# Performance work log

Measured on AMD Instinct MI355X. Metric: run time of the kernel, lower is better.

The kernel has to match this reference:

```python
import jax, jax.numpy as jnp
import numpy as np
import math

N, S, T, D = 4, 2048, 2048, 1024

def setup_inputs() -> dict:
    key = jax.random.key(0)
    ks = jax.random.split(key, 6)
    scale = 1.0 / math.sqrt(D)
    return {
        "query": jax.random.normal(ks[0], (N, S, D), dtype=jnp.float32),
        "key": jax.random.normal(ks[1], (N, T, D), dtype=jnp.float32),
        "value": jax.random.normal(ks[2], (N, T, D), dtype=jnp.float32),
        # causal mask: 1 = attend, 0 = masked out (masked_fill where mask == 0)
        "attn_mask": jnp.tril(jnp.ones((S, T), dtype=jnp.int32)),
        "Wq": jax.random.normal(ks[3], (D, D), dtype=jnp.float32) * scale,
        "Wk": jax.random.normal(ks[4], (D, D), dtype=jnp.float32) * scale,
        "Wv": jax.random.normal(ks[5], (D, D), dtype=jnp.float32) * scale,
    }

def reference(query, key, value, attn_mask, Wq, Wk, Wv):
    # nn.Linear(bias=False): y = x @ W.T
    q = jnp.einsum('nsd,ed->nse', query, Wq)
    k = jnp.einsum('ntd,ed->nte', key, Wk)
    v = jnp.einsum('ntd,ed->nte', value, Wv)
    # scaled dot-product scores [N, S, T]
    dot = jnp.einsum('nse,nte->nst', q, k) / jnp.sqrt(jnp.asarray(D, q.dtype))
    dot = jnp.where(attn_mask == 0, -jnp.inf, dot)
    scores = jax.nn.softmax(dot, axis=-1)
    # dropout is identity in eval mode
    y = jnp.einsum('nst,nte->nse', scores, v)
    return y
```

## Files before the change

kernel.cpp:

```cpp
#include <hip/hip_runtime.h>
#include <math.h>

using u16 = unsigned short;
typedef __attribute__((ext_vector_type(8))) __bf16 bf16x8;
typedef __attribute__((ext_vector_type(4))) float f32x4;
typedef __attribute__((ext_vector_type(4))) float f4v;
typedef __attribute__((ext_vector_type(8))) u16 u16x8;

__device__ __forceinline__ u16 f2bf(float f) {
  unsigned u = __float_as_uint(f);
  u += 0x7fffu + ((u >> 16) & 1u);
  return (u16)(u >> 16);
}

__device__ __forceinline__ void gload16(const void* g, void* l) {
  __builtin_amdgcn_global_load_lds(
      (const __attribute__((address_space(1))) unsigned int*)g,
      (__attribute__((address_space(3))) unsigned int*)l, 16, 0, 0);
}

__global__ __launch_bounds__(256) void cast3_f32_bf16(
    const float* __restrict__ p0, const float* __restrict__ p1,
    const float* __restrict__ p2, u16* __restrict__ out, size_t ostride) {
  int z = blockIdx.z;
  const float* in = (z == 0) ? p0 : (z == 1) ? p1 : p2;
  size_t i = ((size_t)blockIdx.x * 256 + threadIdx.x) * 8;
  f4v a = *reinterpret_cast<const f4v*>(in + i);
  f4v b = *reinterpret_cast<const f4v*>(in + i + 4);
  u16x8 r;
  r[0] = f2bf(a[0]); r[1] = f2bf(a[1]); r[2] = f2bf(a[2]); r[3] = f2bf(a[3]);
  r[4] = f2bf(b[0]); r[5] = f2bf(b[1]); r[6] = f2bf(b[2]); r[7] = f2bf(b[3]);
  *reinterpret_cast<u16x8*>(out + z * ostride + i) = r;
}

__global__ __launch_bounds__(256) void transpose_bf16k(const u16* __restrict__ in,
                                                       u16* __restrict__ out) {
  __shared__ u16 t[64][65];
  int c0 = blockIdx.x * 64, r0 = blockIdx.y * 64;
  size_t zb = (size_t)blockIdx.z * 2048 * 1024;
  const u16* I = in + zb;
  u16* O = out + zb;
  int tx = threadIdx.x & 63, ty = threadIdx.x >> 6;
  #pragma unroll
  for (int i = 0; i < 64; i += 4)
    t[ty + i][tx] = I[(size_t)(r0 + ty + i) * 1024 + c0 + tx];
  __syncthreads();
  #pragma unroll
  for (int i = 0; i < 64; i += 4)
    O[(size_t)(c0 + ty + i) * 2048 + r0 + tx] = t[tx][ty + i];
}

#define BM 128
#define BN 128
#define BK 32

template<typename OutT, int MODE>
__global__ __launch_bounds__(256) void gemm_bt(
    const u16* __restrict__ A, const u16* __restrict__ B, OutT* __restrict__ C,
    int K, int lda, int ldb, int ldc,
    size_t sA, size_t sB, size_t sC, float alpha,
    OutT* __restrict__ C1, OutT* __restrict__ C2) {
  int bn, bm, bz = 0;
  int kEnd = K;
  const u16* Ag;
  const u16* Bg;
  OutT* Cg;

  if (MODE == 3) {
    int h = blockIdx.x;
    int l = (h & 7) * 192 + (h >> 3);
    bn = l & 7;
    int bm192 = l >> 3;
    int which = bm192 >> 6;
    bm = bm192 & 63;
    Ag = A + (size_t)which * sA + (size_t)bm * BM * lda;
    Bg = B + (size_t)which * sB + (size_t)bn * BN * ldb;
    Cg = (which == 0) ? C : (which == 1) ? C1 : C2;
  } else if (MODE == 1) {
    int h = blockIdx.x;
    int l = (h & 7) * 68 + (h >> 3);
    bz = l / 136;
    int t = l % 136;
    bm = (int)((sqrtf(8.f * (float)t + 1.f) - 1.f) * 0.5f);
    while ((bm + 1) * (bm + 2) / 2 <= t) ++bm;
    while (bm * (bm + 1) / 2 > t) --bm;
    bn = t - bm * (bm + 1) / 2;
    Ag = A + sA * bz + (size_t)bm * BM * lda;
    Bg = B + sB * bz + (size_t)bn * BN * ldb;
    Cg = C + sC * bz;
  } else {
    int l = blockIdx.x;
    bm = 15 - (l >> 5);
    int rest = l & 31;
    bz = rest >> 3;
    bn = rest & 7;
    kEnd = (K < (bm + 1) * BM) ? K : (bm + 1) * BM;
    Ag = A + sA * bz + (size_t)bm * BM * lda;
    Bg = B + sB * bz + (size_t)bn * BN * ldb;
    Cg = C + sC * bz;
  }

  __shared__ __align__(16) u16 As[2][BM * BK];
  __shared__ __align__(16) u16 Bs[2][BN * BK];

  const int tid = threadIdx.x;
  const int lane = tid & 63, wave = tid >> 6;
  const int wr = wave >> 1, wc = wave & 1;

  const int ch0 = wave, ch1 = wave + 4;
  const int e0 = ch0 * 512 + lane * 8, e1 = ch1 * 512 + lane * 8;
  const int r0 = e0 >> 5, c0 = e0 & 31, r1 = e1 >> 5, c1 = e1 & 31;
  const u16* a0 = Ag + (size_t)r0 * lda + c0;
  const u16* a1 = Ag + (size_t)r1 * lda + c1;
  const u16* b0 = Bg + (size_t)r0 * ldb + c0;
  const u16* b1 = Bg + (size_t)r1 * ldb + c1;

  f32x4 acc[4][4] = {};

  const int fr = lane & 15, kq = (lane >> 4) * 8;
  const int nt = kEnd / BK;

  gload16(a0, &As[0][ch0 * 512]);
  gload16(a1, &As[0][ch1 * 512]);
  gload16(b0, &Bs[0][ch0 * 512]);
  gload16(b1, &Bs[0][ch1 * 512]);
  __syncthreads();

  for (int t = 0; t < nt; ++t) {
    const int cur = t & 1;
    if (t + 1 < nt) {
      const int k0 = (t + 1) * BK;
      gload16(a0 + k0, &As[cur ^ 1][ch0 * 512]);
      gload16(a1 + k0, &As[cur ^ 1][ch1 * 512]);
      gload16(b0 + k0, &Bs[cur ^ 1][ch0 * 512]);
      gload16(b1 + k0, &Bs[cur ^ 1][ch1 * 512]);
    }
    bf16x8 af[4], bfv[4];
    #pragma unroll
    for (int m = 0; m < 4; ++m)
      af[m] = *reinterpret_cast<const bf16x8*>(&As[cur][(wr * 64 + m * 16 + fr) * BK + kq]);
    #pragma unroll
    for (int n = 0; n < 4; ++n)
      bfv[n] = *reinterpret_cast<const bf16x8*>(&Bs[cur][(wc * 64 + n * 16 + fr) * BK + kq]);
    #pragma unroll
    for (int m = 0; m < 4; ++m)
      #pragma unroll
      for (int n = 0; n < 4; ++n)
        acc[m][n] = __builtin_amdgcn_mfma_f32_16x16x32_bf16(af[m], bfv[n], acc[m][n], 0, 0, 0);
    __syncthreads();
  }

  const int row0 = bm * BM + wr * 64 + (lane >> 4) * 4;
  const int col0 = bn * BN + wc * 64 + fr;
  #pragma unroll
  for (int m = 0; m < 4; ++m)
    #pragma unroll
    for (int n = 0; n < 4; ++n) {
      #pragma unroll
      for (int j = 0; j < 4; ++j) {
        float val = acc[m][n][j] * alpha;
        size_t idx = (size_t)(row0 + m * 16 + j) * ldc + (col0 + n * 16);
        if constexpr (sizeof(OutT) == 2) Cg[idx] = f2bf(val);
        else Cg[idx] = val;
      }
    }
}

__global__ __launch_bounds__(256) void softmax_causal(float* __restrict__ sc) {
  int r = blockIdx.x;
  int s = r & 2047;
  float* row = sc + (size_t)r * 2048;
  int tid = threadIdx.x;
  int t0 = tid * 8;
  f4v x0 = {-1e30f, -1e30f, -1e30f, -1e30f};
  f4v x1 = {-1e30f, -1e30f, -1e30f, -1e30f};
  if (t0 <= s)     x0 = reinterpret_cast<const f4v*>(row)[tid * 2];
  if (t0 + 4 <= s) x1 = reinterpret_cast<const f4v*>(row)[tid * 2 + 1];
  float v[8] = {x0[0], x0[1], x0[2], x0[3], x1[0], x1[1], x1[2], x1[3]};
  float mx = -1e30f;
  #pragma unroll
  for (int j = 0; j < 8; ++j) {
    v[j] = ((t0 + j) <= s) ? v[j] : -1e30f;
    mx = fmaxf(mx, v[j]);
  }
  #pragma unroll
  for (int o = 32; o; o >>= 1) mx = fmaxf(mx, __shfl_xor(mx, o, 64));
  __shared__ float red[8];
  if ((tid & 63) == 0) red[tid >> 6] = mx;
  __syncthreads();
  mx = fmaxf(fmaxf(red[0], red[1]), fmaxf(red[2], red[3]));
  float p[8];
  float sum = 0.f;
  #pragma unroll
  for (int j = 0; j < 8; ++j) {
    p[j] = ((t0 + j) <= s) ? __expf(v[j] - mx) : 0.f;
    sum += p[j];
  }
  #pragma unroll
  for (int o = 32; o; o >>= 1) sum += __shfl_xor(sum, o, 64);
  if ((tid & 63) == 0) red[4 + (tid >> 6)] = sum;
  __syncthreads();
  sum = red[4] + red[5] + red[6] + red[7];
  float inv = 1.0f / sum;
  u16x8 o8;
  #pragma unroll
  for (int j = 0; j < 8; ++j) o8[j] = f2bf(p[j] * inv);
  if (t0 <= (s | 127))
    reinterpret_cast<u16x8*>(row)[tid] = o8;
}

extern "C" void kernel_launch(void* const* d_in, const int* in_sizes, int n_in,
                              void* d_out, int out_size, void* d_ws, size_t ws_size,
                              hipStream_t stream) {
  const float* q  = (const float*)d_in[0];
  const float* k  = (const float*)d_in[1];
  const float* v  = (const float*)d_in[2];
  const float* Wq = (const float*)d_in[4];
  const float* Wk = (const float*)d_in[5];
  const float* Wv = (const float*)d_in[6];
  float* out = (float*)d_out;
  char* ws = (char*)d_ws;

  const size_t MB = 1024ull * 1024ull;
  u16* qb  = (u16*)(ws + 0 * MB);
  u16* wqb = (u16*)(ws + 48 * MB);
  u16* Vp  = (u16*)(ws + 54 * MB);
  u16* Vt  = (u16*)(ws + 70 * MB);
  u16* Kp  = (u16*)(ws + 86 * MB);
  u16* Qp  = (u16*)(ws + 102 * MB);
  float* sc = (float*)ws;

  cast3_f32_bf16<<<dim3(4096, 1, 3), 256, 0, stream>>>(q, k, v, qb, 8ull * MB);
  cast3_f32_bf16<<<dim3(512, 1, 3), 256, 0, stream>>>(Wq, Wk, Wv, wqb, 1ull * MB);

  gemm_bt<u16, 3><<<1536, 256, 0, stream>>>(
      qb, wqb, Qp, 1024, 1024, 1024, 1024,
      8ull * MB, 1ull * MB, 0, 1.0f, Kp, Vp);

  transpose_bf16k<<<dim3(16, 32, 4), 256, 0, stream>>>(Vp, Vt);

  gemm_bt<float, 1><<<544, 256, 0, stream>>>(
      Qp, Kp, sc, 1024, 1024, 1024, 2048,
      (size_t)2048 * 1024, (size_t)2048 * 1024, (size_t)2048 * 2048, 0.03125f,
      nullptr, nullptr);

  softmax_causal<<<8192, 256, 0, stream>>>(sc);

  gemm_bt<float, 2><<<512, 256, 0, stream>>>(
      (u16*)ws, Vt, out, 2048, 4096, 2048, 1024,
      (size_t)2048 * 4096, (size_t)1024 * 2048, (size_t)2048 * 1024, 1.0f,
      nullptr, nullptr);
}
```

Baseline: 187.3 us.

## Add 256x256-tile 8-wave GEMM with swizzled LDS for projection and QK^T

Adds a new GEMM kernel with 256x256 output tiles, 512 threads, and BK=64. It uses XOR-swizzled LDS layout, staggered direct-to-LDS prefetch of A and B across the four sub-phases, explicit barriers and waitcnt, and s_setprio around the MFMA bursts. The QKV projection and the causal QK^T score GEMM switch to this kernel, with far fewer, larger blocks. The goal is higher arithmetic intensity and less LDS and global traffic per FLOP. The costs are 128KB of LDS, high register pressure, and coarser causal tiles that compute more of the masked work on the diagonal.

```diff
diff --git a/kernel.cpp b/kernel.cpp
--- a/kernel.cpp
+++ b/kernel.cpp
@@ -18,6 +18,15 @@
       (const __attribute__((address_space(1))) unsigned int*)g,
       (__attribute__((address_space(3))) unsigned int*)l, 16, 0, 0);
 }
+
+__device__ __forceinline__ f32x4 MF(bf16x8 a, bf16x8 b, f32x4 c) {
+  return __builtin_amdgcn_mfma_f32_16x16x32_bf16(a, b, c, 0, 0, 0);
+}
+
+#define BARX() __builtin_amdgcn_s_barrier()
+#define LGKM0() asm volatile("s_waitcnt lgkmcnt(0)" ::: "memory")
+#define VMW4() asm volatile("s_waitcnt vmcnt(4)" ::: "memory")
+#define VMW0() asm volatile("s_waitcnt vmcnt(0)" ::: "memory")
 
 __global__ __launch_bounds__(256) void cast3_f32_bf16(
     const float* __restrict__ p0, const float* __restrict__ p1,
@@ -50,6 +59,188 @@
     O[(size_t)(c0 + ty + i) * 2048 + r0 + tx] = t[tx][ty + i];
 }
 
+template<typename OutT, int MODE>
+__global__ __launch_bounds__(512, 2) void gemm256(
+    const u16* __restrict__ A, const u16* __restrict__ B, OutT* __restrict__ C,
+    int K, int lda, int ldb, int ldc, size_t sA, size_t sB, size_t sC,
+    float alpha, OutT* __restrict__ C1, OutT* __restrict__ C2) {
+  int bm, bn, bz = 0, cm;
+  const u16 *Ag, *Bg;
+  OutT* Cg;
+  if (MODE == 0) {
+    int h = blockIdx.x;
+    int l = (h & 7) * 48 + (h >> 3);
+    bn = l & 3;
+    bm = l >> 2;
+    int which = bm >> 5;
+    cm = bm & 31;
+    Ag = A + (size_t)bm * 256 * lda;
+    Bg = B + (size_t)which * sB + (size_t)bn * 256 * ldb;
+    Cg = (which == 0) ? C : (which == 1) ? C1 : C2;
+  } else {
+    int h = blockIdx.x;
+    int l = (h & 7) * 18 + (h >> 3);
+    bz = l / 36;
+    int tt = l % 36;
+    bm = (int)((sqrtf(8.f * (float)tt + 1.f) - 1.f) * 0.5f);
+    while ((bm + 1) * (bm + 2) / 2 <= tt) ++bm;
+    while (bm * (bm + 1) / 2 > tt) --bm;
+    bn = tt - bm * (bm + 1) / 2;
+    cm = bm;
+    Ag = A + sA * bz + (size_t)bm * 256 * lda;
+    Bg = B + sB * bz + (size_t)bn * 256 * ldb;
+    Cg = C + sC * bz;
+  }
+
+  __shared__ __align__(16) char sm[131072];
+
+  const int tid = threadIdx.x;
+  const int lane = tid & 63, wv = tid >> 6;
+  const int wr = wv >> 2, wc = wv & 3;
+  const int fr = lane & 15, hi = lane >> 4, fr7 = lane & 7;
+  const int l3 = lane >> 3;
+  const int colsw = ((lane & 7) ^ l3) * 8;
+  const int lnx16 = lane * 16;
+
+  const u16 *pA[2][2], *pB[2][2];
+  int ldsA[2][2], ldsB[2][2];
+  #pragma unroll
+  for (int hh = 0; hh < 2; ++hh)
+    #pragma unroll
+    for (int j = 0; j < 2; ++j) {
+      int row = hh * 128 + wv * 8 + j * 64 + l3;
+      pA[hh][j] = Ag + (size_t)row * lda + colsw;
+      pB[hh][j] = Bg + (size_t)row * ldb + colsw;
+      ldsA[hh][j] = hh * 16384 + (wv + j * 8) * 1024 + lnx16;
+      ldsB[hh][j] = 32768 + ldsA[hh][j];
+    }
+
+  const int aBase = wr * 16384 + fr * 128;
+  const int bBase = 32768 + (wc >> 1) * 16384 + ((wc & 1) * 64 + fr) * 128;
+  const int sl0 = (hi ^ fr7) << 4;
+  const int sl1 = ((4 + hi) ^ fr7) << 4;
+
+#define RDA(buf, m, kk) (*(const bf16x8*)((buf) + aBase + (m) * 2048 + ((kk) ? sl1 : sl0)))
+#define RDB(buf, n, kk) (*(const bf16x8*)((buf) + bBase + (n) * 2048 + ((kk) ? sl1 : sl0)))
+
+  f32x4 acc[8][4] = {};
+  const int nt = K >> 6;
+
+  {
+    char* b0 = sm;
+    gload16(pA[0][0], b0 + ldsA[0][0]); gload16(pA[0][1], b0 + ldsA[0][1]);
+    gload16(pA[1][0], b0 + ldsA[1][0]); gload16(pA[1][1], b0 + ldsA[1][1]);
+    gload16(pB[0][0], b0 + ldsB[0][0]); gload16(pB[0][1], b0 + ldsB[0][1]);
+    gload16(pB[1][0], b0 + ldsB[1][0]); gload16(pB[1][1], b0 + ldsB[1][1]);
+    char* b1 = sm + 65536;
+    gload16(pB[0][0] + 64, b1 + ldsB[0][0]); gload16(pB[0][1] + 64, b1 + ldsB[0][1]);
+    gload16(pB[1][0] + 64, b1 + ldsB[1][0]); gload16(pB[1][1] + 64, b1 + ldsB[1][1]);
+  }
+  VMW4();
+  BARX();
+
+  for (int t = 0; t < nt; ++t) {
+    const int cur = t & 1;
+    const char* buf = sm + cur * 65536;
+    char* nbuf = sm + (cur ^ 1) * 65536;
+    char* cbuf = sm + cur * 65536;
+    const bool st1 = (t + 1 < nt), st2 = (t + 2 < nt);
+    bf16x8 bf0[4], bf1[4];
+    bf16x8 a00, a01, a10, a11;
+
+    a00 = RDA(buf, 0, 0); a01 = RDA(buf, 0, 1);
+    a10 = RDA(buf, 1, 0); a11 = RDA(buf, 1, 1);
+    #pragma unroll
+    for (int n = 0; n < 4; ++n) { bf0[n] = RDB(buf, n, 0); bf1[n] = RDB(buf, n, 1); }
+    if (st1) {
+      gload16(pA[0][0] + (t + 1) * 64, nbuf + ldsA[0][0]);
+      gload16(pA[0][1] + (t + 1) * 64, nbuf + ldsA[0][1]);
+    }
+    BARX(); LGKM0();
+    __builtin_amdgcn_s_setprio(1);
+    #pragma unroll
+    for (int n = 0; n < 4; ++n) {
+      acc[0][n] = MF(a00, bf0[n], acc[0][n]);
+      acc[0][n] = MF(a01, bf1[n], acc[0][n]);
+      acc[1][n] = MF(a10, bf0[n], acc[1][n]);
+      acc[1][n] = MF(a11, bf1[n], acc[1][n]);
+    }
+    __builtin_amdgcn_s_setprio(0);
+    BARX();
+
+    a00 = RDA(buf, 2, 0); a01 = RDA(buf, 2, 1);
+    a10 = RDA(buf, 3, 0); a11 = RDA(buf, 3, 1);
+    if (st1) {
+      gload16(pA[1][0] + (t + 1) * 64, nbuf + ldsA[1][0]);
+      gload16(pA[1][1] + (t + 1) * 64, nbuf + ldsA[1][1]);
+    }
+    if (st2) {
+      gload16(pB[0][0] + (t + 2) * 64, cbuf + ldsB[0][0]);
+      gload16(pB[0][1] + (t + 2) * 64, cbuf + ldsB[0][1]);
+    }
+    BARX(); LGKM0();
+    __builtin_amdgcn_s_setprio(1);
+    #pragma unroll
+    for (int n = 0; n < 4; ++n) {
+      acc[2][n] = MF(a00, bf0[n], acc[2][n]);
+      acc[2][n] = MF(a01, bf1[n], acc[2][n]);
+      acc[3][n] = MF(a10, bf0[n], acc[3][n]);
+      acc[3][n] = MF(a11, bf1[n], acc[3][n]);
+    }
+    __builtin_amdgcn_s_setprio(0);
+    BARX();
+
+    a00 = RDA(buf, 4, 0); a01 = RDA(buf, 4, 1);
+    a10 = RDA(buf, 5, 0); a11 = RDA(buf, 5, 1);
+    if (st2) {
+      gload16(pB[1][0] + (t + 2) * 64, cbuf + ldsB[1][0]);
+      gload16(pB[1][1] + (t + 2) * 64, cbuf + ldsB[1][1]);
+    }
+    BARX(); LGKM0();
+    __builtin_amdgcn_s_setprio(1);
+    #pragma unroll
+    for (int n = 0; n < 4; ++n) {
+      acc[4][n] = MF(a00, bf0[n], acc[4][n]);
+      acc[4][n] = MF(a01, bf1[n], acc[4][n]);
+      acc[5][n] = MF(a10, bf0[n], acc[5][n]);
+      acc[5][n] = MF(a11, bf1[n], acc[5][n]);
+    }
+    __builtin_amdgcn_s_setprio(0);
+    BARX();
+
+    a00 = RDA(buf, 6, 0); a01 = RDA(buf, 6, 1);
+    a10 = RDA(buf, 7, 0); a11 = RDA(buf, 7, 1);
+    if (st2) { VMW4(); } else if (st1) { VMW0(); }
+    BARX(); LGKM0();
+    __builtin_amdgcn_s_setprio(1);
+    #pragma unroll
+    for (int n = 0; n < 4; ++n) {
+      acc[6][n] = MF(a00, bf0[n], acc[6][n]);
+      acc[6][n] = MF(a01, bf1[n], acc[6][n]);
+      acc[7][n] = MF(a10, bf0[n], acc[7][n]);
+      acc[7][n] = MF(a11, bf1[n], acc[7][n]);
+    }
+    __builtin_amdgcn_s_setprio(0);
+    BARX();
+  }
+
+  const int row0 = cm * 256 + wr * 128 + hi * 4;
+  const int col0 = bn * 256 + wc * 64 + fr;
+  #pragma unroll
+  for (int m = 0; m < 8; ++m)
+    #pragma unroll
+    for (int n = 0; n < 4; ++n)
+      #pragma unroll
+      for (int j = 0; j < 4; ++j) {
+        float val = acc[m][n][j] * alpha;
+        size_t idx = (size_t)(row0 + m * 16 + j) * ldc + (col0 + n * 16);
+        if constexpr (sizeof(OutT) == 2) Cg[idx] = f2bf(val);
+        else Cg[idx] = val;
+      }
+#undef RDA
+#undef RDB
+}
+
 #define BM 128
 #define BN 128
 #define BK 32
@@ -58,47 +249,17 @@
 __global__ __launch_bounds__(256) void gemm_bt(
     const u16* __restrict__ A, const u16* __restrict__ B, OutT* __restrict__ C,
     int K, int lda, int ldb, int ldc,
-    size_t sA, size_t sB, size_t sC, float alpha,
-    OutT* __restrict__ C1, OutT* __restrict__ C2) {
-  int bn, bm, bz = 0;
-  int kEnd = K;
-  const u16* Ag;
-  const u16* Bg;
-  OutT* Cg;
-
-  if (MODE == 3) {
-    int h = blockIdx.x;
-    int l = (h & 7) * 192 + (h >> 3);
-    bn = l & 7;
-    int bm192 = l >> 3;
-    int which = bm192 >> 6;
-    bm = bm192 & 63;
-    Ag = A + (size_t)which * sA + (size_t)bm * BM * lda;
-    Bg = B + (size_t)which * sB + (size_t)bn * BN * ldb;
-    Cg = (which == 0) ? C : (which == 1) ? C1 : C2;
-  } else if (MODE == 1) {
-    int h = blockIdx.x;
-    int l = (h & 7) * 68 + (h >> 3);
-    bz = l / 136;
-    int t = l % 136;
-    bm = (int)((sqrtf(8.f * (float)t + 1.f) - 1.f) * 0.5f);
-    while ((bm + 1) * (bm + 2) / 2 <= t) ++bm;
-    while (bm * (bm + 1) / 2 > t) --bm;
-    bn = t - bm * (bm + 1) / 2;
-    Ag = A + sA * bz + (size_t)bm * BM * lda;
-    Bg = B + sB * bz + (size_t)bn * BN * ldb;
-    Cg = C + sC * bz;
-  } else {
-    int l = blockIdx.x;
-    bm = 15 - (l >> 5);
-    int rest = l & 31;
-    bz = rest >> 3;
-    bn = rest & 7;
-    kEnd = (K < (bm + 1) * BM) ? K : (bm + 1) * BM;
-    Ag = A + sA * bz + (size_t)bm * BM * lda;
-    Bg = B + sB * bz + (size_t)bn * BN * ldb;
-    Cg = C + sC * bz;
-  }
+    size_t sA, size_t sB, size_t sC, float alpha) {
+  int bn, bm, bz;
+  int l = blockIdx.x;
+  bm = 15 - (l >> 5);
+  int rest = l & 31;
+  bz = rest >> 3;
+  bn = rest & 7;
+  int kEnd = (K < (bm + 1) * BM) ? K : (bm + 1) * BM;
+  const u16* Ag = A + sA * bz + (size_t)bm * BM * lda;
+  const u16* Bg = B + sB * bz + (size_t)bn * BN * ldb;
+  OutT* Cg = C + sC * bz;
 
   __shared__ __align__(16) u16 As[2][BM * BK];
   __shared__ __align__(16) u16 Bs[2][BN * BK];
@@ -146,7 +307,7 @@
     for (int m = 0; m < 4; ++m)
       #pragma unroll
       for (int n = 0; n < 4; ++n)
-        acc[m][n] = __builtin_amdgcn_mfma_f32_16x16x32_bf16(af[m], bfv[n], acc[m][n], 0, 0, 0);
+        acc[m][n] = MF(af[m], bfv[n], acc[m][n]);
     __syncthreads();
   }
 
@@ -233,13 +394,13 @@
   cast3_f32_bf16<<<dim3(4096, 1, 3), 256, 0, stream>>>(q, k, v, qb, 8ull * MB);
   cast3_f32_bf16<<<dim3(512, 1, 3), 256, 0, stream>>>(Wq, Wk, Wv, wqb, 1ull * MB);
 
-  gemm_bt<u16, 3><<<1536, 256, 0, stream>>>(
+  gemm256<u16, 0><<<384, 512, 0, stream>>>(
       qb, wqb, Qp, 1024, 1024, 1024, 1024,
-      8ull * MB, 1ull * MB, 0, 1.0f, Kp, Vp);
+      0, 1048576, 0, 1.0f, Kp, Vp);
 
   transpose_bf16k<<<dim3(16, 32, 4), 256, 0, stream>>>(Vp, Vt);
 
-  gemm_bt<float, 1><<<544, 256, 0, stream>>>(
+  gemm256<float, 1><<<144, 512, 0, stream>>>(
       Qp, Kp, sc, 1024, 1024, 1024, 2048,
       (size_t)2048 * 1024, (size_t)2048 * 1024, (size_t)2048 * 2048, 0.03125f,
       nullptr, nullptr);
@@ -248,6 +409,5 @@
 
   gemm_bt<float, 2><<<512, 256, 0, stream>>>(
       (u16*)ws, Vt, out, 2048, 4096, 2048, 1024,
-      (size_t)2048 * 4096, (size_t)1024 * 2048, (size_t)2048 * 1024, 1.0f,
-      nullptr, nullptr);
-}
+      (size_t)2048 * 4096, (size_t)1024 * 2048, (size_t)2048 * 1024, 1.0f);
+}
```

Result: slower. 192.6 us (+2.8%).

## Fuse fp32-to-bf16 activation cast into the QKV projection GEMM

Applied to the files above, without the earlier changes.

Removes the separate cast pass over the large fp32 query/key/value inputs. The new projection kernel streams fp32 tiles directly into LDS with an XOR swizzle and converts them to bf16 in registers before the MFMA. This avoids writing and re-reading a bf16 copy of the activations, at the cost of twice the LDS footprint and extra global load traffic per A tile inside the GEMM. The workspace layout is rearranged to match, and MODE 3 is dropped from the generic GEMM.

```diff
diff --git a/kernel.cpp b/kernel.cpp
--- a/kernel.cpp
+++ b/kernel.cpp
@@ -17,6 +17,10 @@
   __builtin_amdgcn_global_load_lds(
       (const __attribute__((address_space(1))) unsigned int*)g,
       (__attribute__((address_space(3))) unsigned int*)l, 16, 0, 0);
+}
+
+__device__ __forceinline__ f32x4 MF(bf16x8 a, bf16x8 b, f32x4 c) {
+  return __builtin_amdgcn_mfma_f32_16x16x32_bf16(a, b, c, 0, 0, 0);
 }
 
 __global__ __launch_bounds__(256) void cast3_f32_bf16(
@@ -50,6 +54,98 @@
     O[(size_t)(c0 + ty + i) * 2048 + r0 + tx] = t[tx][ty + i];
 }
 
+__global__ __launch_bounds__(256) void proj_fused(
+    const float* __restrict__ Aq, const float* __restrict__ Ak,
+    const float* __restrict__ Av, const u16* __restrict__ W,
+    u16* __restrict__ Qp, u16* __restrict__ Kp, u16* __restrict__ Vp) {
+  int h = blockIdx.x;
+  int l = (h & 7) * 192 + (h >> 3);
+  int bn = l & 7;
+  int bm192 = l >> 3;
+  int which = bm192 >> 6;
+  int bm = bm192 & 63;
+  const float* Ag = ((which == 0) ? Aq : (which == 1) ? Ak : Av) +
+                    (size_t)bm * 128 * 1024;
+  const u16* Bg = W + (size_t)which * 1048576 + (size_t)bn * 128 * 1024;
+  u16* Cg = (which == 0) ? Qp : (which == 1) ? Kp : Vp;
+
+  __shared__ __align__(16) float Af[2][128 * 32];
+  __shared__ __align__(16) u16  Bs[2][128 * 32];
+
+  const int tid = threadIdx.x, lane = tid & 63, wave = tid >> 6;
+  const int wr = wave >> 1, wc = wave & 1;
+  const int fr = lane & 15, hi = lane >> 4;
+
+  const int arl = lane >> 3;
+  const int acol = ((lane & 7) ^ arl) * 4;
+  const float* ag[4];
+  int alds[4];
+  #pragma unroll
+  for (int j = 0; j < 4; ++j) {
+    int c = wave + j * 4;
+    ag[j] = Ag + (size_t)(c * 8 + arl) * 1024 + acol;
+    alds[j] = c * 256;
+  }
+  const int ch0 = wave, ch1 = wave + 4;
+  const int e0 = ch0 * 512 + lane * 8, e1 = ch1 * 512 + lane * 8;
+  const int br0 = e0 >> 5, bc0 = e0 & 31, br1 = e1 >> 5, bc1 = e1 & 31;
+  const u16* b0 = Bg + (size_t)br0 * 1024 + bc0;
+  const u16* b1 = Bg + (size_t)br1 * 1024 + bc1;
+
+  f32x4 acc[4][4] = {};
+  const int kq = hi * 8;
+
+  #pragma unroll
+  for (int j = 0; j < 4; ++j) gload16(ag[j], &Af[0][alds[j]]);
+  gload16(b0, &Bs[0][ch0 * 512]);
+  gload16(b1, &Bs[0][ch1 * 512]);
+  __syncthreads();
+
+  for (int t = 0; t < 32; ++t) {
+    const int cur = t & 1;
+    if (t + 1 < 32) {
+      const int k0 = (t + 1) * 32;
+      #pragma unroll
+      for (int j = 0; j < 4; ++j) gload16(ag[j] + k0, &Af[cur ^ 1][alds[j]]);
+      gload16(b0 + k0, &Bs[cur ^ 1][ch0 * 512]);
+      gload16(b1 + k0, &Bs[cur ^ 1][ch1 * 512]);
+    }
+    bf16x8 af[4], bfv[4];
+    #pragma unroll
+    for (int m = 0; m < 4; ++m) {
+      int r = wr * 64 + m * 16 + fr;
+      int s0 = (hi * 2) ^ (r & 7);
+      f4v lo = *(const f4v*)&Af[cur][r * 32 + s0 * 4];
+      f4v hh = *(const f4v*)&Af[cur][r * 32 + (s0 ^ 1) * 4];
+      bf16x8 x;
+      x[0] = (__bf16)lo[0]; x[1] = (__bf16)lo[1];
+      x[2] = (__bf16)lo[2]; x[3] = (__bf16)lo[3];
+      x[4] = (__bf16)hh[0]; x[5] = (__bf16)hh[1];
+      x[6] = (__bf16)hh[2]; x[7] = (__bf16)hh[3];
+      af[m] = x;
+    }
+    #pragma unroll
+    for (int n = 0; n < 4; ++n)
+      bfv[n] = *reinterpret_cast<const bf16x8*>(&Bs[cur][(wc * 64 + n * 16 + fr) * 32 + kq]);
+    #pragma unroll
+    for (int m = 0; m < 4; ++m)
+      #pragma unroll
+      for (int n = 0; n < 4; ++n)
+        acc[m][n] = MF(af[m], bfv[n], acc[m][n]);
+    __syncthreads();
+  }
+
+  const int row0 = bm * 128 + wr * 64 + hi * 4;
+  const int col0 = bn * 128 + wc * 64 + fr;
+  #pragma unroll
+  for (int m = 0; m < 4; ++m)
+    #pragma unroll
+    for (int n = 0; n < 4; ++n)
+      #pragma unroll
+      for (int j = 0; j < 4; ++j)
+        Cg[(size_t)(row0 + m * 16 + j) * 1024 + (col0 + n * 16)] = f2bf(acc[m][n][j]);
+}
+
 #define BM 128
 #define BN 128
 #define BK 32
@@ -58,25 +154,10 @@
 __global__ __launch_bounds__(256) void gemm_bt(
     const u16* __restrict__ A, const u16* __restrict__ B, OutT* __restrict__ C,
     int K, int lda, int ldb, int ldc,
-    size_t sA, size_t sB, size_t sC, float alpha,
-    OutT* __restrict__ C1, OutT* __restrict__ C2) {
-  int bn, bm, bz = 0;
+    size_t sA, size_t sB, size_t sC, float alpha) {
+  int bn, bm, bz;
   int kEnd = K;
-  const u16* Ag;
-  const u16* Bg;
-  OutT* Cg;
-
-  if (MODE == 3) {
-    int h = blockIdx.x;
-    int l = (h & 7) * 192 + (h >> 3);
-    bn = l & 7;
-    int bm192 = l >> 3;
-    int which = bm192 >> 6;
-    bm = bm192 & 63;
-    Ag = A + (size_t)which * sA + (size_t)bm * BM * lda;
-    Bg = B + (size_t)which * sB + (size_t)bn * BN * ldb;
-    Cg = (which == 0) ? C : (which == 1) ? C1 : C2;
-  } else if (MODE == 1) {
+  if (MODE == 1) {
     int h = blockIdx.x;
     int l = (h & 7) * 68 + (h >> 3);
     bz = l / 136;
@@ -85,9 +166,6 @@
     while ((bm + 1) * (bm + 2) / 2 <= t) ++bm;
     while (bm * (bm + 1) / 2 > t) --bm;
     bn = t - bm * (bm + 1) / 2;
-    Ag = A + sA * bz + (size_t)bm * BM * lda;
-    Bg = B + sB * bz + (size_t)bn * BN * ldb;
-    Cg = C + sC * bz;
   } else {
     int l = blockIdx.x;
     bm = 15 - (l >> 5);
@@ -95,10 +173,10 @@
     bz = rest >> 3;
     bn = rest & 7;
     kEnd = (K < (bm + 1) * BM) ? K : (bm + 1) * BM;
-    Ag = A + sA * bz + (size_t)bm * BM * lda;
-    Bg = B + sB * bz + (size_t)bn * BN * ldb;
-    Cg = C + sC * bz;
-  }
+  }
+  const u16* Ag = A + sA * bz + (size_t)bm * BM * lda;
+  const u16* Bg = B + sB * bz + (size_t)bn * BN * ldb;
+  OutT* Cg = C + sC * bz;
 
   __shared__ __align__(16) u16 As[2][BM * BK];
   __shared__ __align__(16) u16 Bs[2][BN * BK];
@@ -146,7 +224,7 @@
     for (int m = 0; m < 4; ++m)
       #pragma unroll
       for (int n = 0; n < 4; ++n)
-        acc[m][n] = __builtin_amdgcn_mfma_f32_16x16x32_bf16(af[m], bfv[n], acc[m][n], 0, 0, 0);
+        acc[m][n] = MF(af[m], bfv[n], acc[m][n]);
     __syncthreads();
   }
 
@@ -222,32 +300,27 @@
   char* ws = (char*)d_ws;
 
   const size_t MB = 1024ull * 1024ull;
-  u16* qb  = (u16*)(ws + 0 * MB);
-  u16* wqb = (u16*)(ws + 48 * MB);
-  u16* Vp  = (u16*)(ws + 54 * MB);
-  u16* Vt  = (u16*)(ws + 70 * MB);
-  u16* Kp  = (u16*)(ws + 86 * MB);
-  u16* Qp  = (u16*)(ws + 102 * MB);
   float* sc = (float*)ws;
-
-  cast3_f32_bf16<<<dim3(4096, 1, 3), 256, 0, stream>>>(q, k, v, qb, 8ull * MB);
-  cast3_f32_bf16<<<dim3(512, 1, 3), 256, 0, stream>>>(Wq, Wk, Wv, wqb, 1ull * MB);
-
-  gemm_bt<u16, 3><<<1536, 256, 0, stream>>>(
-      qb, wqb, Qp, 1024, 1024, 1024, 1024,
-      8ull * MB, 1ull * MB, 0, 1.0f, Kp, Vp);
+  u16* Vp  = (u16*)(ws + 0 * MB);
+  u16* wqb = (u16*)(ws + 16 * MB);
+  u16* Vt  = (u16*)(ws + 64 * MB);
+  u16* Kp  = (u16*)(ws + 80 * MB);
+  u16* Qp  = (u16*)(ws + 96 * MB);
+  (void)in_sizes; (void)n_in; (void)out_size; (void)ws_size;
+
+  cast3_f32_bf16<<<dim3(512, 1, 3), 256, 0, stream>>>(Wq, Wk, Wv, wqb, 1048576);
+
+  proj_fused<<<1536, 256, 0, stream>>>(q, k, v, wqb, Qp, Kp, Vp);
 
   transpose_bf16k<<<dim3(16, 32, 4), 256, 0, stream>>>(Vp, Vt);
 
   gemm_bt<float, 1><<<544, 256, 0, stream>>>(
       Qp, Kp, sc, 1024, 1024, 1024, 2048,
-      (size_t)2048 * 1024, (size_t)2048 * 1024, (size_t)2048 * 2048, 0.03125f,
-      nullptr, nullptr);
+      (size_t)2048 * 1024, (size_t)2048 * 1024, (size_t)2048 * 2048, 0.03125f);
 
   softmax_causal<<<8192, 256, 0, stream>>>(sc);
 
   gemm_bt<float, 2><<<512, 256, 0, stream>>>(
       (u16*)ws, Vt, out, 2048, 4096, 2048, 1024,
-      (size_t)2048 * 4096, (size_t)1024 * 2048, (size_t)2048 * 1024, 1.0f,
-      nullptr, nullptr);
-}
+      (size_t)2048 * 4096, (size_t)1024 * 2048, (size_t)2048 * 1024, 1.0f);
+}
```

Result: slower. 237.2 us (+26.6%).

## Store attention scores in bf16 and use 8-wave GEMM blocks

Applied to the files above, without the earlier changes.

The QK^T GEMM now writes scores as bf16 instead of fp32. Softmax reads and writes that bf16 buffer in place, and the PV GEMM reads it with a stride of 2048, which halves the score-matrix traffic. The GEMM kernel also moves to 512 threads (8 waves, each computing a 64x32 sub-tile) over the same 128x128 tile, so each wave holds fewer accumulators and each thread issues fewer loads. Rounding the pre-softmax logits to bf16 adds precision error, and the per-wave MFMA work per LDS read drops.

```diff
diff --git a/kernel.cpp b/kernel.cpp
--- a/kernel.cpp
+++ b/kernel.cpp
@@ -12,11 +12,19 @@
   u += 0x7fffu + ((u >> 16) & 1u);
   return (u16)(u >> 16);
 }
+__device__ __forceinline__ float bf2f(u16 b) {
+  unsigned u = ((unsigned)b) << 16;
+  return __uint_as_float(u);
+}
 
 __device__ __forceinline__ void gload16(const void* g, void* l) {
   __builtin_amdgcn_global_load_lds(
       (const __attribute__((address_space(1))) unsigned int*)g,
       (__attribute__((address_space(3))) unsigned int*)l, 16, 0, 0);
+}
+
+__device__ __forceinline__ f32x4 MF(bf16x8 a, bf16x8 b, f32x4 c) {
+  return __builtin_amdgcn_mfma_f32_16x16x32_bf16(a, b, c, 0, 0, 0);
 }
 
 __global__ __launch_bounds__(256) void cast3_f32_bf16(
@@ -50,33 +58,17 @@
     O[(size_t)(c0 + ty + i) * 2048 + r0 + tx] = t[tx][ty + i];
 }
 
-#define BM 128
-#define BN 128
-#define BK 32
-
 template<typename OutT, int MODE>
-__global__ __launch_bounds__(256) void gemm_bt(
+__global__ __launch_bounds__(512) void gemm_bt8(
     const u16* __restrict__ A, const u16* __restrict__ B, OutT* __restrict__ C,
     int K, int lda, int ldb, int ldc,
     size_t sA, size_t sB, size_t sC, float alpha,
     OutT* __restrict__ C1, OutT* __restrict__ C2) {
   int bn, bm, bz = 0;
   int kEnd = K;
-  const u16* Ag;
-  const u16* Bg;
+  const u16 *Ag, *Bg;
   OutT* Cg;
-
-  if (MODE == 3) {
-    int h = blockIdx.x;
-    int l = (h & 7) * 192 + (h >> 3);
-    bn = l & 7;
-    int bm192 = l >> 3;
-    int which = bm192 >> 6;
-    bm = bm192 & 63;
-    Ag = A + (size_t)which * sA + (size_t)bm * BM * lda;
-    Bg = B + (size_t)which * sB + (size_t)bn * BN * ldb;
-    Cg = (which == 0) ? C : (which == 1) ? C1 : C2;
-  } else if (MODE == 1) {
+  if (MODE == 1) {
     int h = blockIdx.x;
     int l = (h & 7) * 68 + (h >> 3);
     bz = l / 136;
@@ -85,77 +77,79 @@
     while ((bm + 1) * (bm + 2) / 2 <= t) ++bm;
     while (bm * (bm + 1) / 2 > t) --bm;
     bn = t - bm * (bm + 1) / 2;
-    Ag = A + sA * bz + (size_t)bm * BM * lda;
-    Bg = B + sB * bz + (size_t)bn * BN * ldb;
+    Ag = A + sA * bz + (size_t)bm * 128 * lda;
+    Bg = B + sB * bz + (size_t)bn * 128 * ldb;
     Cg = C + sC * bz;
-  } else {
+  } else if (MODE == 2) {
     int l = blockIdx.x;
     bm = 15 - (l >> 5);
     int rest = l & 31;
     bz = rest >> 3;
     bn = rest & 7;
-    kEnd = (K < (bm + 1) * BM) ? K : (bm + 1) * BM;
-    Ag = A + sA * bz + (size_t)bm * BM * lda;
-    Bg = B + sB * bz + (size_t)bn * BN * ldb;
+    kEnd = (K < (bm + 1) * 128) ? K : (bm + 1) * 128;
+    Ag = A + sA * bz + (size_t)bm * 128 * lda;
+    Bg = B + sB * bz + (size_t)bn * 128 * ldb;
     Cg = C + sC * bz;
-  }
-
-  __shared__ __align__(16) u16 As[2][BM * BK];
-  __shared__ __align__(16) u16 Bs[2][BN * BK];
+  } else {
+    int h = blockIdx.x;
+    int l = (h & 7) * 192 + (h >> 3);
+    bn = l & 7;
+    int bm192 = l >> 3;
+    int which = bm192 >> 6;
+    bm = bm192 & 63;
+    Ag = A + (size_t)bm192 * 128 * lda;
+    Bg = B + (size_t)which * sB + (size_t)bn * 128 * ldb;
+    Cg = (which == 0) ? C : (which == 1) ? C1 : C2;
+  }
+
+  __shared__ __align__(16) u16 As[2][128 * 32];
+  __shared__ __align__(16) u16 Bs[2][128 * 32];
 
   const int tid = threadIdx.x;
-  const int lane = tid & 63, wave = tid >> 6;
-  const int wr = wave >> 1, wc = wave & 1;
-
-  const int ch0 = wave, ch1 = wave + 4;
-  const int e0 = ch0 * 512 + lane * 8, e1 = ch1 * 512 + lane * 8;
-  const int r0 = e0 >> 5, c0 = e0 & 31, r1 = e1 >> 5, c1 = e1 & 31;
+  const int lane = tid & 63, wv = tid >> 6;
+  const int wr = wv >> 2, wc = wv & 3;
+  const int fr = lane & 15, kq = (lane >> 4) * 8;
+
+  const int e0 = wv * 512 + lane * 8;
+  const int r0 = e0 >> 5, c0 = e0 & 31;
   const u16* a0 = Ag + (size_t)r0 * lda + c0;
-  const u16* a1 = Ag + (size_t)r1 * lda + c1;
   const u16* b0 = Bg + (size_t)r0 * ldb + c0;
-  const u16* b1 = Bg + (size_t)r1 * ldb + c1;
-
-  f32x4 acc[4][4] = {};
-
-  const int fr = lane & 15, kq = (lane >> 4) * 8;
-  const int nt = kEnd / BK;
-
-  gload16(a0, &As[0][ch0 * 512]);
-  gload16(a1, &As[0][ch1 * 512]);
-  gload16(b0, &Bs[0][ch0 * 512]);
-  gload16(b1, &Bs[0][ch1 * 512]);
+
+  f32x4 acc[4][2] = {};
+  const int nt = kEnd / 32;
+
+  gload16(a0, &As[0][wv * 512]);
+  gload16(b0, &Bs[0][wv * 512]);
   __syncthreads();
 
   for (int t = 0; t < nt; ++t) {
     const int cur = t & 1;
     if (t + 1 < nt) {
-      const int k0 = (t + 1) * BK;
-      gload16(a0 + k0, &As[cur ^ 1][ch0 * 512]);
-      gload16(a1 + k0, &As[cur ^ 1][ch1 * 512]);
-      gload16(b0 + k0, &Bs[cur ^ 1][ch0 * 512]);
-      gload16(b1 + k0, &Bs[cur ^ 1][ch1 * 512]);
+      const int k0 = (t + 1) * 32;
+      gload16(a0 + k0, &As[cur ^ 1][wv * 512]);
+      gload16(b0 + k0, &Bs[cur ^ 1][wv * 512]);
     }
-    bf16x8 af[4], bfv[4];
+    bf16x8 af[4], bfv[2];
     #pragma unroll
     for (int m = 0; m < 4; ++m)
-      af[m] = *reinterpret_cast<const bf16x8*>(&As[cur][(wr * 64 + m * 16 + fr) * BK + kq]);
-    #pragma unroll
-    for (int n = 0; n < 4; ++n)
-      bfv[n] = *reinterpret_cast<const bf16x8*>(&Bs[cur][(wc * 64 + n * 16 + fr) * BK + kq]);
+      af[m] = *reinterpret_cast<const bf16x8*>(&As[cur][(wr * 64 + m * 16 + fr) * 32 + kq]);
+    #pragma unroll
+    for (int n = 0; n < 2; ++n)
+      bfv[n] = *reinterpret_cast<const bf16x8*>(&Bs[cur][(wc * 32 + n * 16 + fr) * 32 + kq]);
     #pragma unroll
     for (int m = 0; m < 4; ++m)
       #pragma unroll
-      for (int n = 0; n < 4; ++n)
-        acc[m][n] = __builtin_amdgcn_mfma_f32_16x16x32_bf16(af[m], bfv[n], acc[m][n], 0, 0, 0);
+      for (int n = 0; n < 2; ++n)
+        acc[m][n] = MF(af[m], bfv[n], acc[m][n]);
     __syncthreads();
   }
 
-  const int row0 = bm * BM + wr * 64 + (lane >> 4) * 4;
-  const int col0 = bn * BN + wc * 64 + fr;
+  const int row0 = bm * 128 + wr * 64 + (lane >> 4) * 4;
+  const int col0 = bn * 128 + wc * 32 + fr;
   #pragma unroll
   for (int m = 0; m < 4; ++m)
     #pragma unroll
-    for (int n = 0; n < 4; ++n) {
+    for (int n = 0; n < 2; ++n) {
       #pragma unroll
       for (int j = 0; j < 4; ++j) {
         float val = acc[m][n][j] * alpha;
@@ -166,21 +160,19 @@
     }
 }
 
-__global__ __launch_bounds__(256) void softmax_causal(float* __restrict__ sc) {
+__global__ __launch_bounds__(256) void softmax_causal(u16* __restrict__ sc) {
   int r = blockIdx.x;
   int s = r & 2047;
-  float* row = sc + (size_t)r * 2048;
+  u16* row = sc + (size_t)r * 2048;
   int tid = threadIdx.x;
   int t0 = tid * 8;
-  f4v x0 = {-1e30f, -1e30f, -1e30f, -1e30f};
-  f4v x1 = {-1e30f, -1e30f, -1e30f, -1e30f};
-  if (t0 <= s)     x0 = reinterpret_cast<const f4v*>(row)[tid * 2];
-  if (t0 + 4 <= s) x1 = reinterpret_cast<const f4v*>(row)[tid * 2 + 1];
-  float v[8] = {x0[0], x0[1], x0[2], x0[3], x1[0], x1[1], x1[2], x1[3]};
+  u16x8 raw = {0, 0, 0, 0, 0, 0, 0, 0};
+  if (t0 <= s) raw = *reinterpret_cast<const u16x8*>(row + t0);
+  float v[8];
   float mx = -1e30f;
   #pragma unroll
   for (int j = 0; j < 8; ++j) {
-    v[j] = ((t0 + j) <= s) ? v[j] : -1e30f;
+    v[j] = ((t0 + j) <= s) ? bf2f(raw[j]) : -1e30f;
     mx = fmaxf(mx, v[j]);
   }
   #pragma unroll
@@ -206,7 +198,7 @@
   #pragma unroll
   for (int j = 0; j < 8; ++j) o8[j] = f2bf(p[j] * inv);
   if (t0 <= (s | 127))
-    reinterpret_cast<u16x8*>(row)[tid] = o8;
+    *reinterpret_cast<u16x8*>(row + t0) = o8;
 }
 
 extern "C" void kernel_launch(void* const* d_in, const int* in_sizes, int n_in,
@@ -222,32 +214,33 @@
   char* ws = (char*)d_ws;
 
   const size_t MB = 1024ull * 1024ull;
-  u16* qb  = (u16*)(ws + 0 * MB);
-  u16* wqb = (u16*)(ws + 48 * MB);
-  u16* Vp  = (u16*)(ws + 54 * MB);
-  u16* Vt  = (u16*)(ws + 70 * MB);
-  u16* Kp  = (u16*)(ws + 86 * MB);
-  u16* Qp  = (u16*)(ws + 102 * MB);
-  float* sc = (float*)ws;
+  u16* sc   = (u16*)ws;
+  u16* qb   = (u16*)(ws + 0 * MB);
+  u16* wqb  = (u16*)(ws + 48 * MB);
+  u16* Vp   = (u16*)(ws + 54 * MB);
+  u16* Vt   = (u16*)(ws + 70 * MB);
+  u16* Kp   = (u16*)(ws + 86 * MB);
+  u16* Qp   = (u16*)(ws + 102 * MB);
+  (void)in_sizes; (void)n_in; (void)out_size; (void)ws_size;
 
   cast3_f32_bf16<<<dim3(4096, 1, 3), 256, 0, stream>>>(q, k, v, qb, 8ull * MB);
   cast3_f32_bf16<<<dim3(512, 1, 3), 256, 0, stream>>>(Wq, Wk, Wv, wqb, 1ull * MB);
 
-  gemm_bt<u16, 3><<<1536, 256, 0, stream>>>(
+  gemm_bt8<u16, 3><<<1536, 512, 0, stream>>>(
       qb, wqb, Qp, 1024, 1024, 1024, 1024,
-      8ull * MB, 1ull * MB, 0, 1.0f, Kp, Vp);
+      0, 1ull * MB, 0, 1.0f, Kp, Vp);
 
   transpose_bf16k<<<dim3(16, 32, 4), 256, 0, stream>>>(Vp, Vt);
 
-  gemm_bt<float, 1><<<544, 256, 0, stream>>>(
+  gemm_bt8<u16, 1><<<544, 512, 0, stream>>>(
       Qp, Kp, sc, 1024, 1024, 1024, 2048,
       (size_t)2048 * 1024, (size_t)2048 * 1024, (size_t)2048 * 2048, 0.03125f,
       nullptr, nullptr);
 
   softmax_causal<<<8192, 256, 0, stream>>>(sc);
 
-  gemm_bt<float, 2><<<512, 256, 0, stream>>>(
-      (u16*)ws, Vt, out, 2048, 4096, 2048, 1024,
-      (size_t)2048 * 4096, (size_t)1024 * 2048, (size_t)2048 * 1024, 1.0f,
+  gemm_bt8<float, 2><<<512, 512, 0, stream>>>(
+      sc, Vt, out, 2048, 2048, 2048, 1024,
+      (size_t)2048 * 2048, (size_t)1024 * 2048, (size_t)2048 * 1024, 1.0f,
       nullptr, nullptr);
 }
```

Result: faster. 179.9 us (-3.9%).
